# Performance work log

Hardware: AMD Instinct MI355X
Metric: run time of the kernel (lower is better)

Reference implementation:

```python
import jax, jax.numpy as jnp
import numpy as np


def setup_inputs() -> dict:
    key = jax.random.key(0)
    ks = jax.random.split(key, 7)
    B, T, I, H, O = 256, 1024, 3, 128, 3
    s = 1.0 / np.sqrt(H)  # torch nn.RNN/Linear default init scale
    return {
        "inputs": jax.random.normal(ks[0], (B, T, I), dtype=jnp.float32),
        "W_ih": jax.random.uniform(ks[1], (H, I), jnp.float32, -s, s),
        "W_hh": jax.random.uniform(ks[2], (H, H), jnp.float32, -s, s),
        "b_ih": jax.random.uniform(ks[3], (H,), jnp.float32, -s, s),
        "b_hh": jax.random.uniform(ks[4], (H,), jnp.float32, -s, s),
        "h0": jnp.zeros((1, H), dtype=jnp.float32),  # learned initial hidden (init zeros)
        "W_out": jax.random.uniform(ks[5], (O, H), jnp.float32, -s, s),
        "b_out": jax.random.uniform(ks[6], (O,), jnp.float32, -s, s),
    }


def reference(inputs, W_ih, W_hh, b_ih, b_hh, h0, W_out, b_out):
    # inputs: [B, T, I]; Elman RNN with tanh, batch_first, single layer.
    B = inputs.shape[0]
    # Precompute input projection for all timesteps: [T, B, H]
    x_proj = jnp.einsum('bti,hi->tbh', inputs, W_ih) + b_ih + b_hh
    h_init = jnp.broadcast_to(h0, (B, h0.shape[1]))

    def step(h, xp):
        h_new = jnp.tanh(xp + h @ W_hh.T)
        return h_new, h_new

    _, hiddens_tbh = jax.lax.scan(step, h_init, x_proj)
    hiddens = jnp.transpose(hiddens_tbh, (1, 0, 2))  # [B, T, H]
    output = jnp.einsum('bth,oh->bto', hiddens, W_out) + b_out  # [B, T, O]
    return output, hiddens
```

## Files before the change

kernel.cpp:

```cpp
#include <hip/hip_runtime.h>

#define BB 256
#define TT 1024
#define II 3
#define HH 128
#define OO 3
#define NT 576

#if __has_builtin(__builtin_amdgcn_exp2f)
#define EXP2F __builtin_amdgcn_exp2f
#else
#define EXP2F exp2f
#endif
#if __has_builtin(__builtin_amdgcn_rcpf)
#define RCPF __builtin_amdgcn_rcpf
#else
#define RCPF(x) (1.0f / (x))
#endif

__device__ __forceinline__ float fast_tanh(float x) {
    float e = EXP2F(x * 2.885390081777927f);
    return 1.0f - 2.0f * RCPF(e + 1.0f);
}

__device__ __forceinline__ void bar_lds() {
    asm volatile("s_waitcnt lgkmcnt(0)\n\ts_barrier" ::: "memory");
}

template <int CTRL>
__device__ __forceinline__ float dpp_add(float p) {
    return p + __uint_as_float(__builtin_amdgcn_update_dpp(
        0, (int)__float_as_uint(p), CTRL, 0xF, 0xF, true));
}
#define DPP_XOR1 0xB1
#define DPP_XOR2 0x4E
#define DPP_HALF_MIRROR 0x141

__device__ __forceinline__ float quad_reduce(float p) {
    p = dpp_add<DPP_XOR1>(p);
    p = dpp_add<DPP_XOR2>(p);
    return p;
}

__global__ __launch_bounds__(NT) void rnn_kernel(
    const float* __restrict__ x,
    const float* __restrict__ Wih,
    const float* __restrict__ Whh,
    const float* __restrict__ bih,
    const float* __restrict__ bhh,
    const float* __restrict__ h0,
    const float* __restrict__ Wout,
    const float* __restrict__ bout,
    float* __restrict__ out,
    float* __restrict__ hid)
{
    __shared__ __align__(16) float4 xs[TT];
    __shared__ __align__(16) float hbuf[2][HH];
    __shared__ __align__(16) float psum[2][OO * 16];

    const int tid = threadIdx.x;
    const int b = blockIdx.x;

    const float* xb = x + (size_t)b * TT * II;
    for (int idx = tid; idx < TT * II; idx += NT) {
        int t = idx / 3;
        int c = idx - t * 3;
        ((float*)&xs[t])[c] = xb[idx];
    }
    if (tid < HH) hbuf[0][tid] = h0[tid];

    if (tid < 512) {
        const int lane = tid & 63;
        const int wv   = tid >> 6;
        const int g    = lane >> 3;
        const int s    = lane & 7;
        const int o0   = (wv * 8 + g) * 2;
        const int swz  = s >> 1;

        float w0[16], w1[16];
        {
            const float* r0 = Whh + (size_t)o0 * HH + s * 16;
            const float* r1 = r0 + HH;
#pragma unroll
            for (int j = 0; j < 4; j++) {
                const int jj = (j + swz) & 3;
#pragma unroll
                for (int c = 0; c < 4; c++) {
                    w0[4 * j + c] = r0[4 * jj + c];
                    w1[4 * j + c] = r1[4 * jj + c];
                }
            }
        }
        const float wi00 = Wih[o0 * II + 0], wi01 = Wih[o0 * II + 1],
                    wi02 = Wih[o0 * II + 2];
        const float wi10 = Wih[(o0 + 1) * II + 0], wi11 = Wih[(o0 + 1) * II + 1],
                    wi12 = Wih[(o0 + 1) * II + 2];
        const float bias0 = bih[o0] + bhh[o0];
        const float bias1 = bih[o0 + 1] + bhh[o0 + 1];

        bar_lds();

        auto cstep = [&](int t, const float* hcur, float* hnext) {
            float a0, a1;
            if (s == 0) {
                float4 xv = xs[t];
                a0 = fmaf(xv.x, wi00, bias0);
                a0 = fmaf(xv.y, wi01, a0);
                a0 = fmaf(xv.z, wi02, a0);
                a1 = fmaf(xv.x, wi10, bias1);
                a1 = fmaf(xv.y, wi11, a1);
                a1 = fmaf(xv.z, wi12, a1);
            } else {
                a0 = 0.f;
                a1 = 0.f;
            }
            const float4* hr = (const float4*)hcur + s * 4;
#pragma unroll
            for (int j = 0; j < 4; j++) {
                const int jj = (j + swz) & 3;
                float4 hh = hr[jj];
                a0 = fmaf(w0[4 * j + 0], hh.x, a0);
                a0 = fmaf(w0[4 * j + 1], hh.y, a0);
                a0 = fmaf(w0[4 * j + 2], hh.z, a0);
                a0 = fmaf(w0[4 * j + 3], hh.w, a0);
                a1 = fmaf(w1[4 * j + 0], hh.x, a1);
                a1 = fmaf(w1[4 * j + 1], hh.y, a1);
                a1 = fmaf(w1[4 * j + 2], hh.z, a1);
                a1 = fmaf(w1[4 * j + 3], hh.w, a1);
            }
            a0 = dpp_add<DPP_XOR1>(a0);
            a0 = dpp_add<DPP_XOR2>(a0);
            a0 = dpp_add<DPP_HALF_MIRROR>(a0);
            a1 = dpp_add<DPP_XOR1>(a1);
            a1 = dpp_add<DPP_XOR2>(a1);
            a1 = dpp_add<DPP_HALF_MIRROR>(a1);
            float th0 = fast_tanh(a0);
            float th1 = fast_tanh(a1);
            if (s == 0) {
                float2 hv;
                hv.x = th0;
                hv.y = th1;
                ((float2*)hnext)[wv * 8 + g] = hv;
            }
            bar_lds();
        };

        for (int t = 0; t < TT; t += 2) {
            cstep(t, hbuf[0], hbuf[1]);
            cstep(t + 1, hbuf[1], hbuf[0]);
        }
    } else {
        const int L = tid - 512;
        const float w00 = Wout[0 * HH + 2 * L], w01 = Wout[0 * HH + 2 * L + 1];
        const float w10 = Wout[1 * HH + 2 * L], w11 = Wout[1 * HH + 2 * L + 1];
        const float w20 = Wout[2 * HH + 2 * L], w21 = Wout[2 * HH + 2 * L + 1];
        const float bL = (L == 0) ? bout[0] : (L == 1) ? bout[1]
                       : (L == 2) ? bout[2] : 0.f;
        float* ob = out + (size_t)b * TT * OO;
        float* hb = hid + (size_t)b * TT * HH;
        const int q = L >> 2;
        const bool qlead = (L & 3) == 0;

        bar_lds();

        auto sstep = [&](int t, const float* hcur, float* psA, const float* psB) {
            if (t >= 1) {
                const float2 hv = ((const float2*)hcur)[L];
                ((float2*)(hb + (size_t)(t - 1) * HH))[L] = hv;
                float p0 = fmaf(hv.x, w00, hv.y * w01);
                float p1 = fmaf(hv.x, w10, hv.y * w11);
                float p2 = fmaf(hv.x, w20, hv.y * w21);
                p0 = quad_reduce(p0);
                p1 = quad_reduce(p1);
                p2 = quad_reduce(p2);
                if (qlead) {
                    psA[0 * 16 + q] = p0;
                    psA[1 * 16 + q] = p1;
                    psA[2 * 16 + q] = p2;
                }
            }
            if (t >= 2 && L < OO) {
                const float4* pp = (const float4*)(psB + L * 16);
                float4 u0 = pp[0], u1 = pp[1], u2 = pp[2], u3 = pp[3];
                float s0 = ((u0.x + u0.y) + (u0.z + u0.w)) +
                           ((u1.x + u1.y) + (u1.z + u1.w));
                float s1 = ((u2.x + u2.y) + (u2.z + u2.w)) +
                           ((u3.x + u3.y) + (u3.z + u3.w));
                ob[(size_t)(t - 2) * OO + L] = s0 + s1 + bL;
            }
            bar_lds();
        };

        for (int t = 0; t < TT; t += 2) {
            sstep(t, hbuf[0], psum[0], psum[1]);
            sstep(t + 1, hbuf[1], psum[1], psum[0]);
        }

        {
            const float2 hv = ((const float2*)hbuf[0])[L];
            ((float2*)(hb + (size_t)(TT - 1) * HH))[L] = hv;
            float p0 = fmaf(hv.x, w00, hv.y * w01);
            float p1 = fmaf(hv.x, w10, hv.y * w11);
            float p2 = fmaf(hv.x, w20, hv.y * w21);
            p0 = quad_reduce(p0);
            p1 = quad_reduce(p1);
            p2 = quad_reduce(p2);
            if (qlead) {
                psum[0][0 * 16 + q] = p0;
                psum[0][1 * 16 + q] = p1;
                psum[0][2 * 16 + q] = p2;
            }
            if (L < OO) {
                const float4* pp = (const float4*)(psum[1] + L * 16);
                float4 u0 = pp[0], u1 = pp[1], u2 = pp[2], u3 = pp[3];
                float s0 = ((u0.x + u0.y) + (u0.z + u0.w)) +
                           ((u1.x + u1.y) + (u1.z + u1.w));
                float s1 = ((u2.x + u2.y) + (u2.z + u2.w)) +
                           ((u3.x + u3.y) + (u3.z + u3.w));
                ob[(size_t)(TT - 2) * OO + L] = s0 + s1 + bL;
                const float4* pq = (const float4*)(psum[0] + L * 16);
                float4 v0 = pq[0], v1 = pq[1], v2 = pq[2], v3 = pq[3];
                float r0 = ((v0.x + v0.y) + (v0.z + v0.w)) +
                           ((v1.x + v1.y) + (v1.z + v1.w));
                float r1 = ((v2.x + v2.y) + (v2.z + v2.w)) +
                           ((v3.x + v3.y) + (v3.z + v3.w));
                ob[(size_t)(TT - 1) * OO + L] = r0 + r1 + bL;
            }
        }
    }
}

extern "C" void kernel_launch(void* const* d_in, const int* in_sizes, int n_in,
                              void* d_out, int out_size, void* d_ws, size_t ws_size,
                              hipStream_t stream) {
    const float* x    = (const float*)d_in[0];
    const float* Wih  = (const float*)d_in[1];
    const float* Whh  = (const float*)d_in[2];
    const float* bih  = (const float*)d_in[3];
    const float* bhh  = (const float*)d_in[4];
    const float* h0   = (const float*)d_in[5];
    const float* Wout = (const float*)d_in[6];
    const float* bout = (const float*)d_in[7];

    float* out = (float*)d_out;
    float* hid = out + (size_t)BB * TT * OO;

    rnn_kernel<<<BB, NT, 0, stream>>>(x, Wih, Whh, bih, bhh, h0, Wout, bout, out, hid);
}
```

Before: 468.8 us.

## Compute four outputs per 16-lane group with permuted hidden-state layout

```diff
diff --git a/kernel.cpp b/kernel.cpp
--- a/kernel.cpp
+++ b/kernel.cpp
@@ -34,13 +34,16 @@
 }
 #define DPP_XOR1 0xB1
 #define DPP_XOR2 0x4E
-#define DPP_HALF_MIRROR 0x141
+#define DPP_HMIR 0x141
+#define DPP_MIRR 0x140
 
 __device__ __forceinline__ float quad_reduce(float p) {
     p = dpp_add<DPP_XOR1>(p);
     p = dpp_add<DPP_XOR2>(p);
     return p;
 }
+
+__device__ __forceinline__ int psi(int c) { return (c >> 1) | ((c & 1) << 4); }
 
 __global__ __launch_bounds__(NT) void rnn_kernel(
     const float* __restrict__ x,
@@ -67,81 +70,70 @@
         int c = idx - t * 3;
         ((float*)&xs[t])[c] = xb[idx];
     }
-    if (tid < HH) hbuf[0][tid] = h0[tid];
+    if (tid < HH) hbuf[0][4 * psi(tid >> 2) + (tid & 3)] = h0[tid];
 
     if (tid < 512) {
         const int lane = tid & 63;
         const int wv   = tid >> 6;
-        const int g    = lane >> 3;
-        const int s    = lane & 7;
-        const int o0   = (wv * 8 + g) * 2;
-        const int swz  = s >> 1;
-
-        float w0[16], w1[16];
-        {
-            const float* r0 = Whh + (size_t)o0 * HH + s * 16;
-            const float* r1 = r0 + HH;
+        const int og   = lane >> 4;
+        const int s    = lane & 15;
+        const int obase = wv * 16 + og * 4;
+        const int u    = s ^ (15 * (s >> 3));
+
+        float w[4][8];
 #pragma unroll
-            for (int j = 0; j < 4; j++) {
-                const int jj = (j + swz) & 3;
-#pragma unroll
-                for (int c = 0; c < 4; c++) {
-                    w0[4 * j + c] = r0[4 * jj + c];
-                    w1[4 * j + c] = r1[4 * jj + c];
-                }
-            }
-        }
-        const float wi00 = Wih[o0 * II + 0], wi01 = Wih[o0 * II + 1],
-                    wi02 = Wih[o0 * II + 2];
-        const float wi10 = Wih[(o0 + 1) * II + 0], wi11 = Wih[(o0 + 1) * II + 1],
-                    wi12 = Wih[(o0 + 1) * II + 2];
-        const float bias0 = bih[o0] + bhh[o0];
-        const float bias1 = bih[o0 + 1] + bhh[o0 + 1];
+        for (int j = 0; j < 4; ++j) {
+            const float* wr = Whh + (size_t)(obase + j) * HH + 8 * s;
+            float4 v1 = ((const float4*)wr)[0];
+            float4 v2 = ((const float4*)wr)[1];
+            w[j][0] = v1.x; w[j][1] = v1.y; w[j][2] = v1.z; w[j][3] = v1.w;
+            w[j][4] = v2.x; w[j][5] = v2.y; w[j][6] = v2.z; w[j][7] = v2.w;
+        }
+        const int ru = obase + (u & 3);
+        const float wiu0 = Wih[ru * II + 0];
+        const float wiu1 = Wih[ru * II + 1];
+        const float wiu2 = Wih[ru * II + 2];
+        const float biasu = bih[ru] + bhh[ru];
+        const int wpos = 4 * psi(wv * 4 + og) + s;
 
         bar_lds();
 
         auto cstep = [&](int t, const float* hcur, float* hnext) {
-            float a0, a1;
-            if (s == 0) {
-                float4 xv = xs[t];
-                a0 = fmaf(xv.x, wi00, bias0);
-                a0 = fmaf(xv.y, wi01, a0);
-                a0 = fmaf(xv.z, wi02, a0);
-                a1 = fmaf(xv.x, wi10, bias1);
-                a1 = fmaf(xv.y, wi11, a1);
-                a1 = fmaf(xv.z, wi12, a1);
-            } else {
-                a0 = 0.f;
-                a1 = 0.f;
-            }
-            const float4* hr = (const float4*)hcur + s * 4;
-#pragma unroll
-            for (int j = 0; j < 4; j++) {
-                const int jj = (j + swz) & 3;
-                float4 hh = hr[jj];
-                a0 = fmaf(w0[4 * j + 0], hh.x, a0);
-                a0 = fmaf(w0[4 * j + 1], hh.y, a0);
-                a0 = fmaf(w0[4 * j + 2], hh.z, a0);
-                a0 = fmaf(w0[4 * j + 3], hh.w, a0);
-                a1 = fmaf(w1[4 * j + 0], hh.x, a1);
-                a1 = fmaf(w1[4 * j + 1], hh.y, a1);
-                a1 = fmaf(w1[4 * j + 2], hh.z, a1);
-                a1 = fmaf(w1[4 * j + 3], hh.w, a1);
-            }
-            a0 = dpp_add<DPP_XOR1>(a0);
-            a0 = dpp_add<DPP_XOR2>(a0);
-            a0 = dpp_add<DPP_HALF_MIRROR>(a0);
-            a1 = dpp_add<DPP_XOR1>(a1);
-            a1 = dpp_add<DPP_XOR2>(a1);
-            a1 = dpp_add<DPP_HALF_MIRROR>(a1);
-            float th0 = fast_tanh(a0);
-            float th1 = fast_tanh(a1);
-            if (s == 0) {
-                float2 hv;
-                hv.x = th0;
-                hv.y = th1;
-                ((float2*)hnext)[wv * 8 + g] = hv;
-            }
+            float4 h1 = ((const float4*)hcur)[s];
+            float4 h2 = ((const float4*)hcur)[16 + s];
+            float a0e = 0.f, a0o = 0.f, a1e = 0.f, a1o = 0.f;
+            float a2e = 0.f, a2o = 0.f, a3e = 0.f, a3o = 0.f;
+            a0e = fmaf(w[0][0], h1.x, a0e); a0o = fmaf(w[0][1], h1.y, a0o);
+            a0e = fmaf(w[0][2], h1.z, a0e); a0o = fmaf(w[0][3], h1.w, a0o);
+            a0e = fmaf(w[0][4], h2.x, a0e); a0o = fmaf(w[0][5], h2.y, a0o);
+            a0e = fmaf(w[0][6], h2.z, a0e); a0o = fmaf(w[0][7], h2.w, a0o);
+            a1e = fmaf(w[1][0], h1.x, a1e); a1o = fmaf(w[1][1], h1.y, a1o);
+            a1e = fmaf(w[1][2], h1.z, a1e); a1o = fmaf(w[1][3], h1.w, a1o);
+            a1e = fmaf(w[1][4], h2.x, a1e); a1o = fmaf(w[1][5], h2.y, a1o);
+            a1e = fmaf(w[1][6], h2.z, a1e); a1o = fmaf(w[1][7], h2.w, a1o);
+            a2e = fmaf(w[2][0], h1.x, a2e); a2o = fmaf(w[2][1], h1.y, a2o);
+            a2e = fmaf(w[2][2], h1.z, a2e); a2o = fmaf(w[2][3], h1.w, a2o);
+            a2e = fmaf(w[2][4], h2.x, a2e); a2o = fmaf(w[2][5], h2.y, a2o);
+            a2e = fmaf(w[2][6], h2.z, a2e); a2o = fmaf(w[2][7], h2.w, a2o);
+            a3e = fmaf(w[3][0], h1.x, a3e); a3o = fmaf(w[3][1], h1.y, a3o);
+            a3e = fmaf(w[3][2], h1.z, a3e); a3o = fmaf(w[3][3], h1.w, a3o);
+            a3e = fmaf(w[3][4], h2.x, a3e); a3o = fmaf(w[3][5], h2.y, a3o);
+            a3e = fmaf(w[3][6], h2.z, a3e); a3o = fmaf(w[3][7], h2.w, a3o);
+            float a0 = a0e + a0o, a1 = a1e + a1o;
+            float a2 = a2e + a2o, a3 = a3e + a3o;
+            a0 = dpp_add<DPP_XOR1>(a0); a0 = dpp_add<DPP_XOR2>(a0); a0 = dpp_add<DPP_HMIR>(a0);
+            a1 = dpp_add<DPP_XOR1>(a1); a1 = dpp_add<DPP_XOR2>(a1); a1 = dpp_add<DPP_HMIR>(a1);
+            a2 = dpp_add<DPP_XOR1>(a2); a2 = dpp_add<DPP_XOR2>(a2); a2 = dpp_add<DPP_HMIR>(a2);
+            a3 = dpp_add<DPP_XOR1>(a3); a3 = dpp_add<DPP_XOR2>(a3); a3 = dpp_add<DPP_HMIR>(a3);
+            float asel = a0;
+            asel = (u == 1) ? a1 : asel;
+            asel = (u == 2) ? a2 : asel;
+            asel = (u == 3) ? a3 : asel;
+            asel = dpp_add<DPP_MIRR>(asel);
+            float4 xv = xs[t];
+            float xp = fmaf(xv.z, wiu2, fmaf(xv.y, wiu1, fmaf(xv.x, wiu0, biasu)));
+            float val = fast_tanh(asel + xp);
+            if (s < 4) hnext[wpos] = val;
             bar_lds();
         };
 
@@ -160,12 +152,13 @@
         float* hb = hid + (size_t)b * TT * HH;
         const int q = L >> 2;
         const bool qlead = (L & 3) == 0;
+        const int fpos = 4 * psi(L >> 1) + 2 * (L & 1);
 
         bar_lds();
 
         auto sstep = [&](int t, const float* hcur, float* psA, const float* psB) {
             if (t >= 1) {
-                const float2 hv = ((const float2*)hcur)[L];
+                const float2 hv = *(const float2*)(hcur + fpos);
                 ((float2*)(hb + (size_t)(t - 1) * HH))[L] = hv;
                 float p0 = fmaf(hv.x, w00, hv.y * w01);
                 float p1 = fmaf(hv.x, w10, hv.y * w11);
@@ -197,7 +190,7 @@
         }
 
         {
-            const float2 hv = ((const float2*)hbuf[0])[L];
+            const float2 hv = *(const float2*)(&hbuf[0][0] + fpos);
             ((float2*)(hb + (size_t)(TT - 1) * HH))[L] = hv;
             float p0 = fmaf(hv.x, w00, hv.y * w01);
             float p1 = fmaf(hv.x, w10, hv.y * w11);
```

New measurement: 470.1 us. Within noise of the previous version (+0.3%).
